# Kernel optimization log

Measured on AMD Instinct MI355X. Metric: run time of the kernel, lower is better.

## Reference

```python
import jax, jax.numpy as jnp
import numpy as np

N = 50000        # nodes
E = 1600000      # edges (before self loops)
IN = 256         # in_channels
C = 32           # hidden_channels (per head)
H = 4            # heads
OUT = 64         # out_channels
NEG_SLOPE = 0.2  # PyG GATConv default


def setup_inputs() -> dict:
    key = jax.random.key(0)
    ks = jax.random.split(key, 8)
    x = jax.random.normal(ks[0], (N, IN), dtype=jnp.float32)
    edge_index = jax.random.randint(ks[1], (2, E), 0, N, dtype=jnp.int64)
    s = 0.05
    W = jax.random.normal(ks[2], (IN, H * C), dtype=jnp.float32) * s
    att_src = jax.random.normal(ks[3], (H, C), dtype=jnp.float32) * s
    att_dst = jax.random.normal(ks[4], (H, C), dtype=jnp.float32) * s
    bias = jnp.zeros((H * C,), dtype=jnp.float32)
    lin_W = jax.random.normal(ks[5], (H * C, OUT), dtype=jnp.float32) * s
    lin_b = jnp.zeros((OUT,), dtype=jnp.float32)
    return {"x": x, "edge_index": edge_index, "W": W, "att_src": att_src,
            "att_dst": att_dst, "bias": bias, "lin_W": lin_W, "lin_b": lin_b}


def reference(x, edge_index, W, att_src, att_dst, bias, lin_W, lin_b):
    # Linear transform per head: [N, H, C]
    h = (x @ W).reshape(N, H, C)
    # Per-node attention halves (PyG GATConv): [N, H]
    a_src = jnp.einsum('nhc,hc->nh', h, att_src)
    a_dst = jnp.einsum('nhc,hc->nh', h, att_dst)
    # Add self loops (PyG default add_self_loops=True)
    loop = jnp.arange(N, dtype=edge_index.dtype)
    src = jnp.concatenate([edge_index[0], loop])  # message source j
    dst = jnp.concatenate([edge_index[1], loop])  # message target i
    # Edge attention logits: LeakyReLU(a_src[j] + a_dst[i])  -> [E+N, H]
    e = jax.nn.leaky_relu(a_src[src] + a_dst[dst], negative_slope=NEG_SLOPE)
    # Segment softmax over incoming edges of each destination node
    emax = jax.lax.stop_gradient(jax.ops.segment_max(e, dst, num_segments=N))
    emax = jnp.where(jnp.isfinite(emax), emax, 0.0)
    ex = jnp.exp(e - emax[dst])
    denom = jax.ops.segment_sum(ex, dst, num_segments=N)
    alpha = ex / denom[dst]  # [E+N, H]; self loops guarantee denom > 0
    # Weighted scatter-sum of source features: [N, H, C]
    msg = alpha[:, :, None] * h[src]
    agg = jax.ops.segment_sum(msg, dst, num_segments=N)
    out = agg.reshape(N, H * C) + bias  # concat heads + bias
    out = jax.nn.elu(out)
    return out @ lin_W + lin_b
```

## Files before the change

kernel.cpp:

```cpp
#include <hip/hip_runtime.h>
#include <cstdint>
#include <cstddef>

#define N_NODES 50000
#define N_EDGES 1600000
#define TOT_E   (N_EDGES + N_NODES)
#define IN_DIM  256
#define HC      128
#define NHEAD   4
#define OUT_DIM 64

#define SHIFT   7
#define BSZ     128
#define NBUK    ((N_NODES + BSZ - 1) / BSZ)
#define CHUNK   2048
#define EPT     8
#define NCHUNK  ((TOT_E + CHUNK - 1) / CHUNK)
#define CAP     6144
#define QCAP    1792

#define XPAD 264
#define HPAD 132
#define K1_NB ((N_NODES + 63) / 64)

#define W2_GEMM_BLK ((HC * IN_DIM) / 256)
#define W2_LIN_BLK  ((OUT_DIM * HC) / 256)

typedef __attribute__((ext_vector_type(8))) short bf16x8;
typedef __attribute__((ext_vector_type(4))) float f32x4;
typedef __attribute__((ext_vector_type(4))) unsigned short u16x4;

static __device__ __forceinline__ uint16_t f2bf(float f) {
    uint32_t u = __float_as_uint(f);
    uint32_t r = (u + 0x7fffu + ((u >> 16) & 1u)) >> 16;
    return (uint16_t)r;
}
static __device__ __forceinline__ float bf_lo(uint32_t u) {
    return __uint_as_float(u << 16);
}
static __device__ __forceinline__ float bf_hi(uint32_t u) {
    return __uint_as_float(u & 0xffff0000u);
}

__global__ __launch_bounds__(256) void w2bf(const float* __restrict__ W,
                                            const float* __restrict__ linW,
                                            uint16_t* __restrict__ wt,
                                            uint16_t* __restrict__ lwt,
                                            int* __restrict__ gcur) {
    if (blockIdx.x < W2_GEMM_BLK) {
        int idx = blockIdx.x * 256 + threadIdx.x;
        int n = idx >> 8, k = idx & 255;
        wt[idx] = f2bf(W[(size_t)k * HC + n]);
        if (idx < NBUK) gcur[idx] = 0;
    } else {
        int idx = (blockIdx.x - W2_GEMM_BLK) * 256 + threadIdx.x;
        int n = idx >> 7, k = idx & 127;
        float w = linW[(size_t)k * OUT_DIM + n];
        uint16_t h = f2bf(w);
        float hf = __uint_as_float((uint32_t)h << 16);
        lwt[idx] = h;
        lwt[OUT_DIM * HC + idx] = f2bf(w - hf);
    }
}

__global__ __launch_bounds__(256) void k1p3(const float* __restrict__ x,
                                            const uint16_t* __restrict__ wt,
                                            const float* __restrict__ att_src,
                                            const float* __restrict__ att_dst,
                                            uint16_t* __restrict__ hb,
                                            float* __restrict__ a_src,
                                            float* __restrict__ a_dst,
                                            const int* __restrict__ ei,
                                            int* __restrict__ gcur,
                                            uint32_t* __restrict__ binned) {
    __shared__ char smem[64 * 528];
    __shared__ float att_s[HC], att_d[HC];
    const int tid = threadIdx.x;

    if (blockIdx.x < K1_NB) {
        uint16_t* xs = (uint16_t*)smem;
        float*    hs = (float*)smem;
        const int wave = tid >> 6;
        const int lane = tid & 63;
        const int m    = lane & 15;
        const int q    = lane >> 4;
        const int row0 = blockIdx.x * 64;

        if (tid < HC) { att_s[tid] = att_src[tid]; att_d[tid] = att_dst[tid]; }

        for (int i = tid * 4; i < 64 * IN_DIM; i += 1024) {
            int r = i >> 8, c = i & 255;
            int gr = row0 + r;
            float4 v = make_float4(0.f, 0.f, 0.f, 0.f);
            if (gr < N_NODES) v = *(const float4*)(x + (size_t)gr * IN_DIM + c);
            uint32_t lo = (uint32_t)f2bf(v.x) | ((uint32_t)f2bf(v.y) << 16);
            uint32_t hi = (uint32_t)f2bf(v.z) | ((uint32_t)f2bf(v.w) << 16);
            *(uint2*)(xs + r * XPAD + c) = make_uint2(lo, hi);
        }
        __syncthreads();

        f32x4 acc[8];
        #pragma unroll
        for (int t = 0; t < 8; ++t) acc[t] = (f32x4){0.f, 0.f, 0.f, 0.f};

        const int arow = wave * 16 + m;
        #pragma unroll
        for (int ks = 0; ks < IN_DIM; ks += 32) {
            bf16x8 a = *(const bf16x8*)(xs + arow * XPAD + ks + q * 8);
            #pragma unroll
            for (int t = 0; t < 8; ++t) {
                bf16x8 b = *(const bf16x8*)(wt + (size_t)(t * 16 + m) * IN_DIM + ks + q * 8);
                acc[t] = __builtin_amdgcn_mfma_f32_16x16x32_bf16(a, b, acc[t], 0, 0, 0);
            }
        }
        __syncthreads();

        #pragma unroll
        for (int t = 0; t < 8; ++t)
            #pragma unroll
            for (int r = 0; r < 4; ++r)
                hs[(wave * 16 + q * 4 + r) * HPAD + t * 16 + m] = acc[t][r];
        __syncthreads();

        for (int i = tid * 4; i < 64 * HC; i += 1024) {
            int r = i >> 7, c = i & 127;
            if (row0 + r < N_NODES) {
                float4 v = *(const float4*)(hs + r * HPAD + c);
                uint32_t lo = (uint32_t)f2bf(v.x) | ((uint32_t)f2bf(v.y) << 16);
                uint32_t hi = (uint32_t)f2bf(v.z) | ((uint32_t)f2bf(v.w) << 16);
                *(uint2*)(hb + (size_t)(row0 + r) * HC + c) = make_uint2(lo, hi);
            }
        }
        {
            int r = tid >> 2, hd = tid & 3;
            if (row0 + r < N_NODES) {
                float s = 0.f, d = 0.f;
                #pragma unroll
                for (int j = 0; j < 32; ++j) {
                    float v = hs[r * HPAD + hd * 32 + j];
                    s = fmaf(v, att_s[hd * 32 + j], s);
                    d = fmaf(v, att_d[hd * 32 + j], d);
                }
                a_src[(row0 + r) * NHEAD + hd] = s;
                a_dst[(row0 + r) * NHEAD + hd] = d;
            }
        }
    } else {
        int* hist = (int*)smem;
        int* lcur = hist + NBUK;
        for (int i = tid; i < NBUK; i += 256) hist[i] = 0;
        __syncthreads();

        uint32_t wreg[EPT];
        const int base = (blockIdx.x - K1_NB) * CHUNK;
        #pragma unroll
        for (int k = 0; k < EPT; ++k) {
            int e = base + k * 256 + tid;
            uint32_t word = 0xFFFFFFFFu;
            if (e < TOT_E) {
                int src, dst;
                if (e < N_EDGES) { src = ei[e]; dst = ei[N_EDGES + e]; }
                else             { src = e - N_EDGES; dst = src; }
                int b = dst >> SHIFT;
                word = (uint32_t)src | ((uint32_t)(dst & (BSZ - 1)) << 16)
                     | ((uint32_t)b << 23);
                atomicAdd(&hist[b], 1);
            }
            wreg[k] = word;
        }
        __syncthreads();
        for (int i = tid; i < NBUK; i += 256) {
            int c = hist[i];
            lcur[i] = c ? atomicAdd(&gcur[i], c) : 0;
        }
        __syncthreads();
        #pragma unroll
        for (int k = 0; k < EPT; ++k) {
            uint32_t word = wreg[k];
            if (word != 0xFFFFFFFFu) {
                int b = (int)(word >> 23);
                int pos = atomicAdd(&lcur[b], 1);
                if (pos < CAP) binned[(size_t)b * CAP + pos] = word;
            }
        }
    }
}

__global__ __launch_bounds__(512) void q4_agg(const uint32_t* __restrict__ binned,
                                              const int* __restrict__ gcur,
                                              const uint32_t* __restrict__ hb32,
                                              const float* __restrict__ a_src,
                                              const float* __restrict__ a_dst,
                                              const float* __restrict__ bias,
                                              uint32_t* __restrict__ actb) {
    __shared__ uint32_t ewb[QCAP];
    __shared__ uint16_t ew2[QCAP * 2];
    __shared__ int ncnt[32], nbeg[32], ncur[32];
    __shared__ int tot;
    const int b   = blockIdx.x >> 2;
    const int sub = blockIdx.x & 3;
    const int tid = threadIdx.x;

    int cnt = gcur[b];
    if (cnt > CAP) cnt = CAP;
    if (tid == 0) tot = 0;
    if (tid < 32) ncnt[tid] = 0;
    __syncthreads();

    const uint32_t* bb = binned + (size_t)b * CAP;
    for (int i = tid; i < cnt; i += 512) {
        uint32_t word = bb[i];
        int dl = (word >> 16) & 127;
        if ((dl >> 5) == sub) {
            int pos = atomicAdd(&tot, 1);
            if (pos < QCAP) ewb[pos] = word;
            atomicAdd(&ncnt[dl & 31], 1);
        }
    }
    __syncthreads();
    int T = tot;
    if (T > QCAP) T = QCAP;

    if (tid < 32) {
        int v  = ncnt[tid];
        int v4 = (v + 3) & ~3;
        int inc = v4;
        #pragma unroll
        for (int d = 1; d < 32; d <<= 1) {
            int t = __shfl_up(inc, d, 64);
            if (tid >= d) inc += t;
        }
        nbeg[tid] = inc - v4;
        ncur[tid] = inc - v4;
    }
    __syncthreads();
    for (int i = tid; i < T; i += 512) {
        uint32_t word = ewb[i];
        int ln  = (word >> 16) & 31;
        int pos = atomicAdd(&ncur[ln], 1);
        ew2[pos] = (uint16_t)(word & 0xFFFFu);
    }
    __syncthreads();

    const int wave = tid >> 6;
    const int lane = tid & 63;
    const int g    = lane >> 4;
    const int sl   = lane & 15;
    const int head = sl >> 2;
    const char*  hb8 = (const char*)hb32 + sl * 16;
    const float* ash = a_src + head;
    const float4 bA = *(const float4*)(bias + sl * 8);
    const float4 bB = *(const float4*)(bias + sl * 8 + 4);

    const int ln   = wave * 4 + g;
    const int node = b * BSZ + sub * 32 + ln;
    const int myc  = ncnt[ln];
    const int p0   = nbeg[ln];
    int m1   = max(myc, __shfl_xor(myc, 16, 64));
    int maxc = max(m1,  __shfl_xor(m1, 32, 64));
    const float ad = a_dst[min(node, N_NODES - 1) * NHEAD + head];

    float l = 0.f;
    float acc[8];
    #pragma unroll
    for (int j = 0; j < 8; ++j) acc[j] = 0.f;

    for (int i = 0; i < maxc; i += 4) {
        u16x4 sv = *(const u16x4*)(&ew2[p0 + i]);
        const int s0 = sv[0], s1 = sv[1], s2 = sv[2], s3 = sv[3];
        float as0 = ash[s0 * NHEAD];
        float as1 = ash[s1 * NHEAD];
        float as2 = ash[s2 * NHEAD];
        float as3 = ash[s3 * NHEAD];
        uint4 h0 = *(const uint4*)(hb8 + ((uint32_t)s0 << 8));
        uint4 h1 = *(const uint4*)(hb8 + ((uint32_t)s1 << 8));
        uint4 h2 = *(const uint4*)(hb8 + ((uint32_t)s2 << 8));
        uint4 h3 = *(const uint4*)(hb8 + ((uint32_t)s3 << 8));
        float e0 = as0 + ad, e1 = as1 + ad, e2 = as2 + ad, e3 = as3 + ad;
        e0 = fmaxf(e0, 0.2f * e0);
        e1 = fmaxf(e1, 0.2f * e1);
        e2 = fmaxf(e2, 0.2f * e2);
        e3 = fmaxf(e3, 0.2f * e3);
        float w0 = __expf(e0), w1 = __expf(e1);
        float w2 = __expf(e2), w3 = __expf(e3);
        w0 = (i + 0 < myc) ? w0 : 0.f;
        w1 = (i + 1 < myc) ? w1 : 0.f;
        w2 = (i + 2 < myc) ? w2 : 0.f;
        w3 = (i + 3 < myc) ? w3 : 0.f;
        l += (w0 + w1) + (w2 + w3);
        acc[0] = fmaf(w0, bf_lo(h0.x), acc[0]); acc[0] = fmaf(w1, bf_lo(h1.x), acc[0]);
        acc[0] = fmaf(w2, bf_lo(h2.x), acc[0]); acc[0] = fmaf(w3, bf_lo(h3.x), acc[0]);
        acc[1] = fmaf(w0, bf_hi(h0.x), acc[1]); acc[1] = fmaf(w1, bf_hi(h1.x), acc[1]);
        acc[1] = fmaf(w2, bf_hi(h2.x), acc[1]); acc[1] = fmaf(w3, bf_hi(h3.x), acc[1]);
        acc[2] = fmaf(w0, bf_lo(h0.y), acc[2]); acc[2] = fmaf(w1, bf_lo(h1.y), acc[2]);
        acc[2] = fmaf(w2, bf_lo(h2.y), acc[2]); acc[2] = fmaf(w3, bf_lo(h3.y), acc[2]);
        acc[3] = fmaf(w0, bf_hi(h0.y), acc[3]); acc[3] = fmaf(w1, bf_hi(h1.y), acc[3]);
        acc[3] = fmaf(w2, bf_hi(h2.y), acc[3]); acc[3] = fmaf(w3, bf_hi(h3.y), acc[3]);
        acc[4] = fmaf(w0, bf_lo(h0.z), acc[4]); acc[4] = fmaf(w1, bf_lo(h1.z), acc[4]);
        acc[4] = fmaf(w2, bf_lo(h2.z), acc[4]); acc[4] = fmaf(w3, bf_lo(h3.z), acc[4]);
        acc[5] = fmaf(w0, bf_hi(h0.z), acc[5]); acc[5] = fmaf(w1, bf_hi(h1.z), acc[5]);
        acc[5] = fmaf(w2, bf_hi(h2.z), acc[5]); acc[5] = fmaf(w3, bf_hi(h3.z), acc[5]);
        acc[6] = fmaf(w0, bf_lo(h0.w), acc[6]); acc[6] = fmaf(w1, bf_lo(h1.w), acc[6]);
        acc[6] = fmaf(w2, bf_lo(h2.w), acc[6]); acc[6] = fmaf(w3, bf_lo(h3.w), acc[6]);
        acc[7] = fmaf(w0, bf_hi(h0.w), acc[7]); acc[7] = fmaf(w1, bf_hi(h1.w), acc[7]);
        acc[7] = fmaf(w2, bf_hi(h2.w), acc[7]); acc[7] = fmaf(w3, bf_hi(h3.w), acc[7]);
    }

    if (node < N_NODES) {
        const float inv = 1.f / l;
        float o[8];
        o[0] = fmaf(acc[0], inv, bA.x); o[1] = fmaf(acc[1], inv, bA.y);
        o[2] = fmaf(acc[2], inv, bA.z); o[3] = fmaf(acc[3], inv, bA.w);
        o[4] = fmaf(acc[4], inv, bB.x); o[5] = fmaf(acc[5], inv, bB.y);
        o[6] = fmaf(acc[6], inv, bB.z); o[7] = fmaf(acc[7], inv, bB.w);
        #pragma unroll
        for (int j = 0; j < 8; ++j)
            o[j] = (o[j] > 0.f) ? o[j] : (__expf(o[j]) - 1.f);
        uint4 pk;
        pk.x = (uint32_t)f2bf(o[0]) | ((uint32_t)f2bf(o[1]) << 16);
        pk.y = (uint32_t)f2bf(o[2]) | ((uint32_t)f2bf(o[3]) << 16);
        pk.z = (uint32_t)f2bf(o[4]) | ((uint32_t)f2bf(o[5]) << 16);
        pk.w = (uint32_t)f2bf(o[6]) | ((uint32_t)f2bf(o[7]) << 16);
        *(uint4*)(actb + (size_t)node * 64 + sl * 4) = pk;
    }
}

__global__ __launch_bounds__(256) void k7_out(const uint16_t* __restrict__ ab,
                                              const uint16_t* __restrict__ lwt,
                                              const float* __restrict__ linb,
                                              float* __restrict__ out) {
    __shared__ uint16_t as_[64][136];
    const int tid  = threadIdx.x;
    const int row0 = blockIdx.x * 64;

    for (int i = tid; i < 64 * 16; i += 256) {
        int r = i >> 4, cw = i & 15;
        int node = row0 + r;
        uint4 v = make_uint4(0, 0, 0, 0);
        if (node < N_NODES) v = *(const uint4*)(ab + (size_t)node * HC + cw * 8);
        *(uint4*)(&as_[r][cw * 8]) = v;
    }
    __syncthreads();

    const int wave = tid >> 6;
    const int lane = tid & 63;
    const int m    = lane & 15;
    const int q    = lane >> 4;
    const uint16_t* lwlo = lwt + OUT_DIM * HC;

    f32x4 acc[4];
    #pragma unroll
    for (int t = 0; t < 4; ++t) acc[t] = (f32x4){0.f, 0.f, 0.f, 0.f};

    const int arow = wave * 16 + m;
    #pragma unroll
    for (int ks = 0; ks < HC; ks += 32) {
        bf16x8 a = *(const bf16x8*)(&as_[arow][ks + q * 8]);
        #pragma unroll
        for (int t = 0; t < 4; ++t) {
            bf16x8 bh = *(const bf16x8*)(lwt  + (size_t)(t * 16 + m) * HC + ks + q * 8);
            bf16x8 bl = *(const bf16x8*)(lwlo + (size_t)(t * 16 + m) * HC + ks + q * 8);
            acc[t] = __builtin_amdgcn_mfma_f32_16x16x32_bf16(a, bh, acc[t], 0, 0, 0);
            acc[t] = __builtin_amdgcn_mfma_f32_16x16x32_bf16(a, bl, acc[t], 0, 0, 0);
        }
    }

    const int grow = row0 + wave * 16 + q * 4;
    #pragma unroll
    for (int t = 0; t < 4; ++t) {
        const int col = t * 16 + m;
        const float lb = linb[col];
        #pragma unroll
        for (int r = 0; r < 4; ++r)
            if (grow + r < N_NODES)
                out[(size_t)(grow + r) * OUT_DIM + col] = acc[t][r] + lb;
    }
}

extern "C" void kernel_launch(void* const* d_in, const int* in_sizes, int n_in,
                              void* d_out, int out_size, void* d_ws, size_t ws_size,
                              hipStream_t stream) {
    (void)in_sizes; (void)n_in; (void)out_size; (void)ws_size;
    const float* x       = (const float*)d_in[0];
    const int*   ei      = (const int*)d_in[1];
    const float* W       = (const float*)d_in[2];
    const float* att_src = (const float*)d_in[3];
    const float* att_dst = (const float*)d_in[4];
    const float* bias    = (const float*)d_in[5];
    const float* linW    = (const float*)d_in[6];
    const float* linb    = (const float*)d_in[7];
    float*       out     = (float*)d_out;

    char*  ws  = (char*)d_ws;
    size_t off = 0;
    auto alloc = [&](size_t bytes) -> void* {
        void* p = ws + off;
        off += (bytes + 255) & ~(size_t)255;
        return p;
    };
    uint16_t* hb     = (uint16_t*)alloc((size_t)N_NODES * HC * 2);
    uint16_t* wt     = (uint16_t*)alloc((size_t)HC * IN_DIM * 2);
    uint32_t* actb   = (uint32_t*)alloc((size_t)N_NODES * 64 * 4);
    float*    a_src  = (float*)alloc((size_t)N_NODES * NHEAD * 4);
    float*    a_dst  = (float*)alloc((size_t)N_NODES * NHEAD * 4);
    int*      gcur   = (int*)alloc((size_t)NBUK * 4);
    uint32_t* binned = (uint32_t*)alloc((size_t)NBUK * CAP * 4);
    uint16_t* lwt    = (uint16_t*)alloc((size_t)2 * OUT_DIM * HC * 2);

    w2bf<<<W2_GEMM_BLK + W2_LIN_BLK, 256, 0, stream>>>(W, linW, wt, lwt, gcur);
    k1p3<<<K1_NB + NCHUNK, 256, 0, stream>>>(x, wt, att_src, att_dst,
                                             hb, a_src, a_dst,
                                             ei, gcur, binned);
    q4_agg<<<NBUK * 4, 512, 0, stream>>>(binned, gcur, (const uint32_t*)hb,
                                         a_src, a_dst, bias, actb);
    k7_out<<<(N_NODES + 63) / 64, 256, 0, stream>>>((const uint16_t*)actb, lwt,
                                                    linb, out);
}
```

Baseline: 235.5 us.

## Replace bucketed binning with fixed-stride per-node CSR via global atomics

Edge binning into 128-node buckets, with a per-block LDS histogram and a second in-kernel scatter pass in the aggregation kernel, is replaced by a direct per-destination fixed-stride adjacency list (88 slots) filled with global atomicAdd on per-node counters. The aggregation kernel now reads source ids straight from global memory instead of rebuilding per-node lists in LDS. The aim is to cut the two-level bucketing and LDS sorting overhead. In exchange it adds 1.65M contended global atomics, scattered 2-byte global writes, and a zero-fill of the CSR buffer. Any edges past 88 per node are silently dropped, and padding slots are assumed to be zero.

```diff
diff --git a/kernel.cpp b/kernel.cpp
--- a/kernel.cpp
+++ b/kernel.cpp
@@ -10,14 +10,10 @@
 #define NHEAD   4
 #define OUT_DIM 64
 
-#define SHIFT   7
-#define BSZ     128
-#define NBUK    ((N_NODES + BSZ - 1) / BSZ)
+#define STRIDE  88
 #define CHUNK   2048
 #define EPT     8
 #define NCHUNK  ((TOT_E + CHUNK - 1) / CHUNK)
-#define CAP     6144
-#define QCAP    1792
 
 #define XPAD 264
 #define HPAD 132
@@ -25,6 +21,8 @@
 
 #define W2_GEMM_BLK ((HC * IN_DIM) / 256)
 #define W2_LIN_BLK  ((OUT_DIM * HC) / 256)
+#define W2_THREADS  ((W2_GEMM_BLK + W2_LIN_BLK) * 256)
+#define CSR_U32     ((N_NODES * STRIDE) / 2)
 
 typedef __attribute__((ext_vector_type(8))) short bf16x8;
 typedef __attribute__((ext_vector_type(4))) float f32x4;
@@ -46,12 +44,16 @@
                                             const float* __restrict__ linW,
                                             uint16_t* __restrict__ wt,
                                             uint16_t* __restrict__ lwt,
-                                            int* __restrict__ gcur) {
+                                            int* __restrict__ cnt,
+                                            uint32_t* __restrict__ csr32) {
+    const int gidx = blockIdx.x * 256 + threadIdx.x;
+    for (int j = gidx; j < N_NODES; j += W2_THREADS) cnt[j] = 0;
+    for (int j = gidx; j < CSR_U32; j += W2_THREADS) csr32[j] = 0;
+
     if (blockIdx.x < W2_GEMM_BLK) {
         int idx = blockIdx.x * 256 + threadIdx.x;
         int n = idx >> 8, k = idx & 255;
         wt[idx] = f2bf(W[(size_t)k * HC + n]);
-        if (idx < NBUK) gcur[idx] = 0;
     } else {
         int idx = (blockIdx.x - W2_GEMM_BLK) * 256 + threadIdx.x;
         int n = idx >> 7, k = idx & 127;
@@ -71,8 +73,8 @@
                                             float* __restrict__ a_src,
                                             float* __restrict__ a_dst,
                                             const int* __restrict__ ei,
-                                            int* __restrict__ gcur,
-                                            uint32_t* __restrict__ binned) {
+                                            int* __restrict__ cnt,
+                                            uint16_t* __restrict__ csr) {
     __shared__ char smem[64 * 528];
     __shared__ float att_s[HC], att_d[HC];
     const int tid = threadIdx.x;
@@ -146,102 +148,30 @@
             }
         }
     } else {
-        int* hist = (int*)smem;
-        int* lcur = hist + NBUK;
-        for (int i = tid; i < NBUK; i += 256) hist[i] = 0;
-        __syncthreads();
-
-        uint32_t wreg[EPT];
         const int base = (blockIdx.x - K1_NB) * CHUNK;
         #pragma unroll
         for (int k = 0; k < EPT; ++k) {
             int e = base + k * 256 + tid;
-            uint32_t word = 0xFFFFFFFFu;
             if (e < TOT_E) {
                 int src, dst;
                 if (e < N_EDGES) { src = ei[e]; dst = ei[N_EDGES + e]; }
                 else             { src = e - N_EDGES; dst = src; }
-                int b = dst >> SHIFT;
-                word = (uint32_t)src | ((uint32_t)(dst & (BSZ - 1)) << 16)
-                     | ((uint32_t)b << 23);
-                atomicAdd(&hist[b], 1);
+                int pos = atomicAdd(&cnt[dst], 1);
+                if (pos < STRIDE)
+                    csr[(size_t)dst * STRIDE + pos] = (uint16_t)src;
             }
-            wreg[k] = word;
-        }
-        __syncthreads();
-        for (int i = tid; i < NBUK; i += 256) {
-            int c = hist[i];
-            lcur[i] = c ? atomicAdd(&gcur[i], c) : 0;
-        }
-        __syncthreads();
-        #pragma unroll
-        for (int k = 0; k < EPT; ++k) {
-            uint32_t word = wreg[k];
-            if (word != 0xFFFFFFFFu) {
-                int b = (int)(word >> 23);
-                int pos = atomicAdd(&lcur[b], 1);
-                if (pos < CAP) binned[(size_t)b * CAP + pos] = word;
-            }
-        }
-    }
-}
-
-__global__ __launch_bounds__(512) void q4_agg(const uint32_t* __restrict__ binned,
-                                              const int* __restrict__ gcur,
+        }
+    }
+}
+
+__global__ __launch_bounds__(512) void q4_agg(const uint16_t* __restrict__ csr,
+                                              const int* __restrict__ cnt,
                                               const uint32_t* __restrict__ hb32,
                                               const float* __restrict__ a_src,
                                               const float* __restrict__ a_dst,
                                               const float* __restrict__ bias,
                                               uint32_t* __restrict__ actb) {
-    __shared__ uint32_t ewb[QCAP];
-    __shared__ uint16_t ew2[QCAP * 2];
-    __shared__ int ncnt[32], nbeg[32], ncur[32];
-    __shared__ int tot;
-    const int b   = blockIdx.x >> 2;
-    const int sub = blockIdx.x & 3;
-    const int tid = threadIdx.x;
-
-    int cnt = gcur[b];
-    if (cnt > CAP) cnt = CAP;
-    if (tid == 0) tot = 0;
-    if (tid < 32) ncnt[tid] = 0;
-    __syncthreads();
-
-    const uint32_t* bb = binned + (size_t)b * CAP;
-    for (int i = tid; i < cnt; i += 512) {
-        uint32_t word = bb[i];
-        int dl = (word >> 16) & 127;
-        if ((dl >> 5) == sub) {
-            int pos = atomicAdd(&tot, 1);
-            if (pos < QCAP) ewb[pos] = word;
-            atomicAdd(&ncnt[dl & 31], 1);
-        }
-    }
-    __syncthreads();
-    int T = tot;
-    if (T > QCAP) T = QCAP;
-
-    if (tid < 32) {
-        int v  = ncnt[tid];
-        int v4 = (v + 3) & ~3;
-        int inc = v4;
-        #pragma unroll
-        for (int d = 1; d < 32; d <<= 1) {
-            int t = __shfl_up(inc, d, 64);
-            if (tid >= d) inc += t;
-        }
-        nbeg[tid] = inc - v4;
-        ncur[tid] = inc - v4;
-    }
-    __syncthreads();
-    for (int i = tid; i < T; i += 512) {
-        uint32_t word = ewb[i];
-        int ln  = (word >> 16) & 31;
-        int pos = atomicAdd(&ncur[ln], 1);
-        ew2[pos] = (uint16_t)(word & 0xFFFFu);
-    }
-    __syncthreads();
-
+    const int tid  = threadIdx.x;
     const int wave = tid >> 6;
     const int lane = tid & 63;
     const int g    = lane >> 4;
@@ -252,10 +182,11 @@
     const float4 bA = *(const float4*)(bias + sl * 8);
     const float4 bB = *(const float4*)(bias + sl * 8 + 4);
 
-    const int ln   = wave * 4 + g;
-    const int node = b * BSZ + sub * 32 + ln;
-    const int myc  = ncnt[ln];
-    const int p0   = nbeg[ln];
+    const int node = blockIdx.x * 32 + wave * 4 + g;
+    int myc = 0;
+    if (node < N_NODES) myc = min(cnt[node], STRIDE);
+    const uint16_t* crow = csr + (size_t)min(node, N_NODES - 1) * STRIDE;
+
     int m1   = max(myc, __shfl_xor(myc, 16, 64));
     int maxc = max(m1,  __shfl_xor(m1, 32, 64));
     const float ad = a_dst[min(node, N_NODES - 1) * NHEAD + head];
@@ -266,7 +197,7 @@
     for (int j = 0; j < 8; ++j) acc[j] = 0.f;
 
     for (int i = 0; i < maxc; i += 4) {
-        u16x4 sv = *(const u16x4*)(&ew2[p0 + i]);
+        u16x4 sv = *(const u16x4*)(crow + i);
         const int s0 = sv[0], s1 = sv[1], s2 = sv[2], s3 = sv[3];
         float as0 = ash[s0 * NHEAD];
         float as1 = ash[s1 * NHEAD];
@@ -403,16 +334,17 @@
     uint32_t* actb   = (uint32_t*)alloc((size_t)N_NODES * 64 * 4);
     float*    a_src  = (float*)alloc((size_t)N_NODES * NHEAD * 4);
     float*    a_dst  = (float*)alloc((size_t)N_NODES * NHEAD * 4);
-    int*      gcur   = (int*)alloc((size_t)NBUK * 4);
-    uint32_t* binned = (uint32_t*)alloc((size_t)NBUK * CAP * 4);
+    int*      cnt    = (int*)alloc((size_t)N_NODES * 4);
+    uint16_t* csr    = (uint16_t*)alloc((size_t)N_NODES * STRIDE * 2);
     uint16_t* lwt    = (uint16_t*)alloc((size_t)2 * OUT_DIM * HC * 2);
 
-    w2bf<<<W2_GEMM_BLK + W2_LIN_BLK, 256, 0, stream>>>(W, linW, wt, lwt, gcur);
+    w2bf<<<W2_GEMM_BLK + W2_LIN_BLK, 256, 0, stream>>>(W, linW, wt, lwt, cnt,
+                                                       (uint32_t*)csr);
     k1p3<<<K1_NB + NCHUNK, 256, 0, stream>>>(x, wt, att_src, att_dst,
                                              hb, a_src, a_dst,
-                                             ei, gcur, binned);
-    q4_agg<<<NBUK * 4, 512, 0, stream>>>(binned, gcur, (const uint32_t*)hb,
-                                         a_src, a_dst, bias, actb);
+                                             ei, cnt, csr);
+    q4_agg<<<(N_NODES + 31) / 32, 512, 0, stream>>>(csr, cnt, (const uint32_t*)hb,
+                                                    a_src, a_dst, bias, actb);
     k7_out<<<(N_NODES + 63) / 64, 256, 0, stream>>>((const uint16_t*)actb, lwt,
                                                     linb, out);
 }
```

New measurement: 280.1 us. 1.19x slower.

## Split bucket regrouping into separate kernel writing padded per-node CSR rows

Applied to the files above, without the earlier changes.

Adds a rgrp kernel that reads each 128-node bucket once and scatters source indices into fixed-stride (88-entry) per-node rows in global memory, plus per-node counts. The aggregation kernel then reads its rows directly instead of having four blocks each rescan the whole bucket and regroup in shared memory. This removes the 4x redundant bucket reads and the shared-memory regroup work, at the cost of an extra launch and a round trip of the CSR through global memory. Nodes with in-degree above 88 would be truncated, and every row is padded to the full stride.

```diff
diff --git a/kernel.cpp b/kernel.cpp
--- a/kernel.cpp
+++ b/kernel.cpp
@@ -17,7 +17,8 @@
 #define EPT     8
 #define NCHUNK  ((TOT_E + CHUNK - 1) / CHUNK)
 #define CAP     6144
-#define QCAP    1792
+#define STRIDE  88
+#define ROWW    (STRIDE / 2)
 
 #define XPAD 264
 #define HPAD 132
@@ -186,62 +187,50 @@
     }
 }
 
-__global__ __launch_bounds__(512) void q4_agg(const uint32_t* __restrict__ binned,
-                                              const int* __restrict__ gcur,
+__global__ __launch_bounds__(256) void rgrp(const uint32_t* __restrict__ binned,
+                                            const int* __restrict__ gcur,
+                                            uint16_t* __restrict__ csr,
+                                            int* __restrict__ cnt) {
+    __shared__ uint32_t lcsr32[BSZ * ROWW];
+    __shared__ int ncnt[BSZ];
+    const int b   = blockIdx.x;
+    const int tid = threadIdx.x;
+
+    for (int j = tid; j < BSZ * ROWW; j += 256) lcsr32[j] = 0;
+    if (tid < BSZ) ncnt[tid] = 0;
+    __syncthreads();
+
+    int c = gcur[b];
+    if (c > CAP) c = CAP;
+    const uint32_t* bb = binned + (size_t)b * CAP;
+    uint16_t* lcsr16 = (uint16_t*)lcsr32;
+    for (int i = tid; i < c; i += 256) {
+        uint32_t w = bb[i];
+        int dl  = (w >> 16) & (BSZ - 1);
+        int pos = atomicAdd(&ncnt[dl], 1);
+        if (pos < STRIDE) lcsr16[dl * STRIDE + pos] = (uint16_t)(w & 0xFFFFu);
+    }
+    __syncthreads();
+
+    const int node0 = b * BSZ;
+    uint32_t* csr32 = (uint32_t*)csr;
+    for (int j = tid; j < BSZ * ROWW; j += 256) {
+        int r = j / ROWW, w = j - r * ROWW;
+        int node = node0 + r;
+        if (node < N_NODES)
+            csr32[(size_t)node * ROWW + w] = lcsr32[j];
+    }
+    if (tid < BSZ && node0 + tid < N_NODES) cnt[node0 + tid] = ncnt[tid];
+}
+
+__global__ __launch_bounds__(512) void q4_agg(const uint16_t* __restrict__ csr,
+                                              const int* __restrict__ cnt,
                                               const uint32_t* __restrict__ hb32,
                                               const float* __restrict__ a_src,
                                               const float* __restrict__ a_dst,
                                               const float* __restrict__ bias,
                                               uint32_t* __restrict__ actb) {
-    __shared__ uint32_t ewb[QCAP];
-    __shared__ uint16_t ew2[QCAP * 2];
-    __shared__ int ncnt[32], nbeg[32], ncur[32];
-    __shared__ int tot;
-    const int b   = blockIdx.x >> 2;
-    const int sub = blockIdx.x & 3;
-    const int tid = threadIdx.x;
-
-    int cnt = gcur[b];
-    if (cnt > CAP) cnt = CAP;
-    if (tid == 0) tot = 0;
-    if (tid < 32) ncnt[tid] = 0;
-    __syncthreads();
-
-    const uint32_t* bb = binned + (size_t)b * CAP;
-    for (int i = tid; i < cnt; i += 512) {
-        uint32_t word = bb[i];
-        int dl = (word >> 16) & 127;
-        if ((dl >> 5) == sub) {
-            int pos = atomicAdd(&tot, 1);
-            if (pos < QCAP) ewb[pos] = word;
-            atomicAdd(&ncnt[dl & 31], 1);
-        }
-    }
-    __syncthreads();
-    int T = tot;
-    if (T > QCAP) T = QCAP;
-
-    if (tid < 32) {
-        int v  = ncnt[tid];
-        int v4 = (v + 3) & ~3;
-        int inc = v4;
-        #pragma unroll
-        for (int d = 1; d < 32; d <<= 1) {
-            int t = __shfl_up(inc, d, 64);
-            if (tid >= d) inc += t;
-        }
-        nbeg[tid] = inc - v4;
-        ncur[tid] = inc - v4;
-    }
-    __syncthreads();
-    for (int i = tid; i < T; i += 512) {
-        uint32_t word = ewb[i];
-        int ln  = (word >> 16) & 31;
-        int pos = atomicAdd(&ncur[ln], 1);
-        ew2[pos] = (uint16_t)(word & 0xFFFFu);
-    }
-    __syncthreads();
-
+    const int tid  = threadIdx.x;
     const int wave = tid >> 6;
     const int lane = tid & 63;
     const int g    = lane >> 4;
@@ -252,10 +241,11 @@
     const float4 bA = *(const float4*)(bias + sl * 8);
     const float4 bB = *(const float4*)(bias + sl * 8 + 4);
 
-    const int ln   = wave * 4 + g;
-    const int node = b * BSZ + sub * 32 + ln;
-    const int myc  = ncnt[ln];
-    const int p0   = nbeg[ln];
+    const int node = blockIdx.x * 32 + wave * 4 + g;
+    int myc = 0;
+    if (node < N_NODES) myc = min(cnt[node], STRIDE);
+    const uint16_t* crow = csr + (size_t)min(node, N_NODES - 1) * STRIDE;
+
     int m1   = max(myc, __shfl_xor(myc, 16, 64));
     int maxc = max(m1,  __shfl_xor(m1, 32, 64));
     const float ad = a_dst[min(node, N_NODES - 1) * NHEAD + head];
@@ -266,7 +256,7 @@
     for (int j = 0; j < 8; ++j) acc[j] = 0.f;
 
     for (int i = 0; i < maxc; i += 4) {
-        u16x4 sv = *(const u16x4*)(&ew2[p0 + i]);
+        u16x4 sv = *(const u16x4*)(crow + i);
         const int s0 = sv[0], s1 = sv[1], s2 = sv[2], s3 = sv[3];
         float as0 = ash[s0 * NHEAD];
         float as1 = ash[s1 * NHEAD];
@@ -405,14 +395,17 @@
     float*    a_dst  = (float*)alloc((size_t)N_NODES * NHEAD * 4);
     int*      gcur   = (int*)alloc((size_t)NBUK * 4);
     uint32_t* binned = (uint32_t*)alloc((size_t)NBUK * CAP * 4);
+    int*      cnt    = (int*)alloc((size_t)N_NODES * 4);
+    uint16_t* csr    = (uint16_t*)alloc((size_t)N_NODES * STRIDE * 2);
     uint16_t* lwt    = (uint16_t*)alloc((size_t)2 * OUT_DIM * HC * 2);
 
     w2bf<<<W2_GEMM_BLK + W2_LIN_BLK, 256, 0, stream>>>(W, linW, wt, lwt, gcur);
     k1p3<<<K1_NB + NCHUNK, 256, 0, stream>>>(x, wt, att_src, att_dst,
                                              hb, a_src, a_dst,
                                              ei, gcur, binned);
-    q4_agg<<<NBUK * 4, 512, 0, stream>>>(binned, gcur, (const uint32_t*)hb,
-                                         a_src, a_dst, bias, actb);
+    rgrp<<<NBUK, 256, 0, stream>>>(binned, gcur, csr, cnt);
+    q4_agg<<<(N_NODES + 31) / 32, 512, 0, stream>>>(csr, cnt, (const uint32_t*)hb,
+                                                    a_src, a_dst, bias, actb);
     k7_out<<<(N_NODES + 63) / 64, 256, 0, stream>>>((const uint16_t*)actb, lwt,
                                                     linb, out);
 }
```

Result: no change. 235.8 us (+0.1%).
